# Kernel optimization log

Measured on AMD Instinct MI355X. Metric: run time of the kernel, lower is better.

## Reference

```python
import jax, jax.numpy as jnp
import numpy as np


def _rbf_kernel(X, Z, variance, lengthscale):
    # K[n, r] = variance * exp(-||x_n - z_r||^2 / (2 * lengthscale^2))
    x2 = jnp.sum(X * X, axis=-1)[:, None]          # [N, 1]
    z2 = jnp.sum(Z * Z, axis=-1)[None, :]          # [1, R]
    sq = x2 + z2 - 2.0 * (X @ Z.T)                 # [N, R]
    sq = jnp.maximum(sq, 0.0)
    return variance * jnp.exp(-0.5 * sq / (lengthscale * lengthscale))


def setup_inputs() -> dict:
    key = jax.random.key(0)
    ks = jax.random.split(key, 6)
    N, D, S, F, R = 16384, 8, 8, 1024, 2048
    X_star = jax.random.normal(ks[0], (N, D), dtype=jnp.float32)
    ref_points = jax.random.normal(ks[1], (R, D), dtype=jnp.float32)
    omega = jax.random.normal(ks[2], (S, D, F), dtype=jnp.float32)
    two_pi = 2.0 * np.pi
    phase = jax.random.uniform(ks[3], (S, F), dtype=jnp.float32) * two_pi
    feature_weights = jax.random.normal(ks[4], (S, F), dtype=jnp.float32)
    correction_weights = jax.random.normal(ks[5], (S, R), dtype=jnp.float32)
    variance = jnp.ones((), dtype=jnp.float32)
    lengthscale = jnp.ones((), dtype=jnp.float32)
    return {
        "X_star": X_star,
        "ref_points": ref_points,
        "omega": omega,
        "phase": phase,
        "feature_weights": feature_weights,
        "correction_weights": correction_weights,
        "variance": variance,
        "lengthscale": lengthscale,
    }


def reference(X_star, ref_points, omega, phase, feature_weights,
              correction_weights, variance, lengthscale):
    F = omega.shape[-1]
    # RFF prior paths: angles [S, N, F]
    angles = jnp.einsum('nd,sdf->snf', X_star, omega) / lengthscale + phase[:, None, :]
    scale = jnp.sqrt(2.0 * variance / F)
    features = scale * jnp.cos(angles)                       # [S, N, F]
    prior = jnp.sum(features * feature_weights[:, None, :], axis=-1)  # [S, N]
    # Kernel correction term
    K_cross = _rbf_kernel(X_star, ref_points, variance, lengthscale)  # [N, R]
    update = jnp.einsum('nr,sr->sn', K_cross, correction_weights)     # [S, N]
    # mean_fn is None -> zero mean
    mean = jnp.zeros(X_star.shape[0], dtype=X_star.dtype)
    return prior + update + mean[None, :]
```

## Files before the change

kernel.cpp:

```cpp
#include <hip/hip_runtime.h>
#include <math.h>

#ifndef __has_builtin
#define __has_builtin(x) 0
#endif

typedef __attribute__((ext_vector_type(8))) short bf16x8;
typedef __attribute__((ext_vector_type(4))) float f32x4;

__device__ __forceinline__ float fast_fract(float x) {
#if __has_builtin(__builtin_amdgcn_fractf)
    return __builtin_amdgcn_fractf(x);
#else
    return x - floorf(x);
#endif
}
__device__ __forceinline__ float fast_cos2pi(float x) {
#if __has_builtin(__builtin_amdgcn_cosf)
    return __builtin_amdgcn_cosf(x);
#else
    return cosf(x * 6.28318530717958647692f);
#endif
}
__device__ __forceinline__ float fast_exp2(float x) {
#if __has_builtin(__builtin_amdgcn_exp2f)
    return __builtin_amdgcn_exp2f(x);
#else
    return exp2f(x);
#endif
}
__device__ __forceinline__ unsigned short f2bf(float f) {
    unsigned u = __float_as_uint(f);
    return (unsigned short)((u + 0x7FFFu + ((u >> 16) & 1u)) >> 16);
}
__device__ __forceinline__ float bf2f(unsigned short b) {
    return __uint_as_float(((unsigned)b) << 16);
}
__device__ __forceinline__ unsigned packbf(float lo, float hi) {
    return (unsigned)f2bf(lo) | ((unsigned)f2bf(hi) << 16);
}

constexpr int kN = 16384, kD = 8, kS = 8, kF = 1024, kR = 2048;
constexpr float kInv2Pi = 0.15915494309189535f;
constexpr float kLog2e  = 1.4426950408889634f;
constexpr int kWsPrior = 512, kWsZ = 128, kWsCw = 64;
constexpr int kWsTiles = kWsPrior + kWsZ + kWsCw;
constexpr size_t kWsNeed = (size_t)kWsTiles * 64 * 16;

__global__ __launch_bounds__(256)
void prep_kernel(const float* __restrict__ omega, const float* __restrict__ phase,
                 const float* __restrict__ Z, const float* __restrict__ cw,
                 const float* __restrict__ lsp, uint4* __restrict__ ws,
                 float* __restrict__ out)
{
    if (blockIdx.x >= 176) {
        const int zid = (blockIdx.x - 176) * 256 + threadIdx.x;
        float4* o4 = reinterpret_cast<float4*>(out);
        #pragma unroll
        for (int j = 0; j < 4; ++j)
            o4[zid * 4 + j] = (float4){0.f, 0.f, 0.f, 0.f};
        return;
    }
    const int job  = blockIdx.x * 256 + threadIdx.x;
    const int lane = job & 63;
    const int tile = job >> 6;
    const int g = lane >> 4, c = lane & 15;

    const float inv_ls = 1.0f / lsp[0];
    const float m_ang  = kInv2Pi * inv_ls;
    const float L      = kLog2e * inv_ls * inv_ls;

    unsigned short h[8];
    if (tile < kWsPrior) {
        const int s = tile >> 6, ft = tile & 63, f = ft * 16 + c;
        const float* om = omega + s * (kD * kF);
        const float* ph = phase + s * kF;
        #pragma unroll
        for (int j = 0; j < 8; ++j) {
            const int k = g * 8 + j;
            unsigned short v = 0;
            if (k < 16) {
                v = f2bf(om[(k & 7) * kF + f] * m_ang);
            } else if (k < 24) {
                const float w = om[(k - 16) * kF + f] * m_ang;
                v = f2bf(w - bf2f(f2bf(w)));
            } else if (k == 24) {
                v = f2bf(ph[f] * kInv2Pi);
            } else if (k == 25) {
                const float p = ph[f] * kInv2Pi;
                v = f2bf(p - bf2f(f2bf(p)));
            }
            h[j] = v;
        }
    } else if (tile < kWsPrior + kWsZ) {
        const int rt = tile - kWsPrior;
        const int r  = rt * 16 + c;
        const float* zr = Z + r * kD;
        float zz = 0.f;
        #pragma unroll
        for (int d = 0; d < kD; ++d) zz = fmaf(zr[d], zr[d], zz);
        const float ztv = -0.5f * L * zz;
        #pragma unroll
        for (int j = 0; j < 8; ++j) {
            const int k = g * 8 + j;
            unsigned short v = 0;
            if (k < 8) {
                v = f2bf(L * zr[k]);
            } else if (k < 16) {
                v = f2bf(L * zr[k - 8]);
            } else if (k < 24) {
                const float w = L * zr[k - 16];
                v = f2bf(w - bf2f(f2bf(w)));
            } else if (k == 24) {
                v = f2bf(ztv);
            } else if (k == 25) {
                v = f2bf(ztv - bf2f(f2bf(ztv)));
            } else if (k < 28) {
                v = 0x3F80;
            }
            h[j] = v;
        }
    } else {
        const int rb = tile - kWsPrior - kWsZ;
        const int r0 = rb * 32;
        #pragma unroll
        for (int j = 0; j < 8; ++j)
            h[j] = (c < 8) ? f2bf(cw[c * kR + r0 + g * 8 + j]) : (unsigned short)0;
    }
    uint4 w;
    w.x = (unsigned)h[0] | ((unsigned)h[1] << 16);
    w.y = (unsigned)h[2] | ((unsigned)h[3] << 16);
    w.z = (unsigned)h[4] | ((unsigned)h[5] << 16);
    w.w = (unsigned)h[6] | ((unsigned)h[7] << 16);
    ws[tile * 64 + lane] = w;
}

__device__ __forceinline__ bf16x8 build_af_x(const float* __restrict__ X,
                                             int row, int g)
{
    float xv[kD];
    const float4 x0 = *reinterpret_cast<const float4*>(X + row * kD);
    const float4 x1 = *reinterpret_cast<const float4*>(X + row * kD + 4);
    xv[0]=x0.x; xv[1]=x0.y; xv[2]=x0.z; xv[3]=x0.w;
    xv[4]=x1.x; xv[5]=x1.y; xv[6]=x1.z; xv[7]=x1.w;
    bf16x8 af;
    if (g == 1) {
        #pragma unroll
        for (int j = 0; j < 8; ++j)
            af[j] = (short)f2bf(xv[j] - bf2f(f2bf(xv[j])));
    } else {
        #pragma unroll
        for (int j = 0; j < 8; ++j) af[j] = (short)f2bf(xv[j]);
    }
    return af;
}

__global__ __launch_bounds__(256, 6)
void fused_main(const float* __restrict__ X, const float* __restrict__ fw,
                const float* __restrict__ varp, const float* __restrict__ lsp,
                const uint4* __restrict__ wsP, const uint4* __restrict__ wsZ,
                const uint4* __restrict__ wsC, float* __restrict__ out)
{
    __shared__ unsigned b2raw[4][256];
    __shared__ f32x4 red[2][2][2][16];
    const int tid  = threadIdx.x;
    const int lane = tid & 63;
    const int w    = __builtin_amdgcn_readfirstlane(tid >> 6);
    const int c = lane & 15, g = lane >> 4;
    const int bid = blockIdx.x;
    const int btype = bid % 3;

    if (btype != 2) {
        const int pb = (bid / 3) * 2 + btype;
        const int s  = pb & 7;
        const int ng = pb >> 3;
        const int n0 = ng * 128 + w * 32;

        bf16x8 af0, af1;
        if (g == 3) {
            #pragma unroll
            for (int j = 0; j < 8; ++j) { af0[j] = 0; af1[j] = 0; }
            af0[0] = (short)0x3F80; af0[1] = (short)0x3F80;
            af1[0] = (short)0x3F80; af1[1] = (short)0x3F80;
        } else {
            af0 = build_af_x(X, n0 + c, g);
            af1 = build_af_x(X, n0 + 16 + c, g);
        }

        const float scale = sqrtf(2.0f * varp[0] / (float)kF);
        const uint4* bp  = wsP + s * 4096 + lane;
        const float* fwp = fw + s * kF + c;

        float acc[2][4];
        #pragma unroll
        for (int t = 0; t < 2; ++t)
            #pragma unroll
            for (int r = 0; r < 4; ++r) acc[t][r] = 0.f;

        uint4 b0 = bp[0], b1 = bp[64];
        f32x4 pd00, pd01, pd10, pd11;
        {
            const bf16x8 v0 = __builtin_bit_cast(bf16x8, b0);
            const bf16x8 v1 = __builtin_bit_cast(bf16x8, b1);
            pd00 = __builtin_amdgcn_mfma_f32_16x16x32_bf16(af0, v0, (f32x4){0.f,0.f,0.f,0.f}, 0, 0, 0);
            pd01 = __builtin_amdgcn_mfma_f32_16x16x32_bf16(af1, v0, (f32x4){0.f,0.f,0.f,0.f}, 0, 0, 0);
            pd10 = __builtin_amdgcn_mfma_f32_16x16x32_bf16(af0, v1, (f32x4){0.f,0.f,0.f,0.f}, 0, 0, 0);
            pd11 = __builtin_amdgcn_mfma_f32_16x16x32_bf16(af1, v1, (f32x4){0.f,0.f,0.f,0.f}, 0, 0, 0);
        }
        float cf0 = fwp[0], cf1 = fwp[16];
        b0 = bp[128]; b1 = bp[192];

        for (int it = 1; it < 32; ++it) {
            const int nx = (it + 1 < 32) ? it + 1 : it;
            const uint4 p0 = bp[nx * 128];
            const uint4 p1 = bp[nx * 128 + 64];
            const float nf0 = fwp[it * 32];
            const float nf1 = fwp[it * 32 + 16];
            const bf16x8 v0 = __builtin_bit_cast(bf16x8, b0);
            const bf16x8 v1 = __builtin_bit_cast(bf16x8, b1);
            const f32x4 nd00 = __builtin_amdgcn_mfma_f32_16x16x32_bf16(af0, v0, (f32x4){0.f,0.f,0.f,0.f}, 0, 0, 0);
            const f32x4 nd01 = __builtin_amdgcn_mfma_f32_16x16x32_bf16(af1, v0, (f32x4){0.f,0.f,0.f,0.f}, 0, 0, 0);
            const f32x4 nd10 = __builtin_amdgcn_mfma_f32_16x16x32_bf16(af0, v1, (f32x4){0.f,0.f,0.f,0.f}, 0, 0, 0);
            const f32x4 nd11 = __builtin_amdgcn_mfma_f32_16x16x32_bf16(af1, v1, (f32x4){0.f,0.f,0.f,0.f}, 0, 0, 0);
            #pragma unroll
            for (int r = 0; r < 4; ++r) {
                acc[0][r] = fmaf(cf0, fast_cos2pi(fast_fract(pd00[r])), acc[0][r]);
                acc[1][r] = fmaf(cf0, fast_cos2pi(fast_fract(pd01[r])), acc[1][r]);
                acc[0][r] = fmaf(cf1, fast_cos2pi(fast_fract(pd10[r])), acc[0][r]);
                acc[1][r] = fmaf(cf1, fast_cos2pi(fast_fract(pd11[r])), acc[1][r]);
            }
            pd00 = nd00; pd01 = nd01; pd10 = nd10; pd11 = nd11;
            cf0 = nf0; cf1 = nf1;
            b0 = p0; b1 = p1;
        }
        #pragma unroll
        for (int r = 0; r < 4; ++r) {
            acc[0][r] = fmaf(cf0, fast_cos2pi(fast_fract(pd00[r])), acc[0][r]);
            acc[1][r] = fmaf(cf0, fast_cos2pi(fast_fract(pd01[r])), acc[1][r]);
            acc[0][r] = fmaf(cf1, fast_cos2pi(fast_fract(pd10[r])), acc[0][r]);
            acc[1][r] = fmaf(cf1, fast_cos2pi(fast_fract(pd11[r])), acc[1][r]);
        }

        #pragma unroll
        for (int m = 1; m <= 8; m <<= 1)
            #pragma unroll
            for (int t = 0; t < 2; ++t)
                #pragma unroll
                for (int r = 0; r < 4; ++r)
                    acc[t][r] += __shfl_xor(acc[t][r], m);

        if (c == 0) {
            #pragma unroll
            for (int t = 0; t < 2; ++t) {
                float* o = out + s * kN + n0 + t * 16 + g * 4;
                #pragma unroll
                for (int r = 0; r < 4; ++r) atomicAdd(o + r, scale * acc[t][r]);
            }
        }
    } else {
        const int ub   = bid / 3;
        const int tl   = w >> 1, half = w & 1;
        const int n0   = (ub * 2 + tl) * 16;

        const float inv_ls = 1.0f / lsp[0];
        const float L = kLog2e * inv_ls * inv_ls;

        bf16x8 bf1;
        {
            float xv[kD];
            const float4 x0 = *reinterpret_cast<const float4*>(X + (n0 + c) * kD);
            const float4 x1 = *reinterpret_cast<const float4*>(X + (n0 + c) * kD + 4);
            xv[0]=x0.x; xv[1]=x0.y; xv[2]=x0.z; xv[3]=x0.w;
            xv[4]=x1.x; xv[5]=x1.y; xv[6]=x1.z; xv[7]=x1.w;
            if (g == 3) {
                float xx = 0.f;
                #pragma unroll
                for (int d = 0; d < kD; ++d) xx = fmaf(xv[d], xv[d], xx);
                const float xt = -0.5f * L * xx;
                const unsigned short th = f2bf(xt);
                const unsigned short tlw = f2bf(xt - bf2f(th));
                #pragma unroll
                for (int j = 0; j < 8; ++j) bf1[j] = 0;
                bf1[0] = (short)0x3F80; bf1[1] = (short)0x3F80;
                bf1[2] = (short)th;     bf1[3] = (short)tlw;
            } else if (g == 1) {
                #pragma unroll
                for (int j = 0; j < 8; ++j)
                    bf1[j] = (short)f2bf(xv[j] - bf2f(f2bf(xv[j])));
            } else {
                #pragma unroll
                for (int j = 0; j < 8; ++j) bf1[j] = (short)f2bf(xv[j]);
            }
        }

        const int wbase = (g >> 1) * 64 + c * 4 + (g & 1) * 2;
        const int rbase = (g >> 1) * 128 + (g & 1) * 64 + c * 4;
        unsigned* bb = &b2raw[w][0];

        const uint4* zp = wsZ + lane;
        const uint4* cp = wsC + lane;
        const int rb0 = half * 32;

        f32x4 acc = {0.f, 0.f, 0.f, 0.f};
        uint4 za = zp[(rb0 * 2) * 64];
        uint4 zb = zp[(rb0 * 2 + 1) * 64];
        uint4 cf = cp[rb0 * 64];

        for (int i = 0; i < 32; ++i) {
            const int rb = rb0 + i;
            const int rbn = (i < 31) ? rb + 1 : rb;
            const uint4 zan = zp[(rbn * 2) * 64];
            const uint4 zbn = zp[(rbn * 2 + 1) * 64];
            const uint4 cfn = cp[rbn * 64];

            const f32x4 e0 = __builtin_amdgcn_mfma_f32_16x16x32_bf16(
                __builtin_bit_cast(bf16x8, za), bf1, (f32x4){0.f,0.f,0.f,0.f}, 0, 0, 0);
            const f32x4 e1 = __builtin_amdgcn_mfma_f32_16x16x32_bf16(
                __builtin_bit_cast(bf16x8, zb), bf1, (f32x4){0.f,0.f,0.f,0.f}, 0, 0, 0);

            float K0[4], K1[4];
            #pragma unroll
            for (int r = 0; r < 4; ++r) {
                K0[r] = fast_exp2(fminf(e0[r], 0.f));
                K1[r] = fast_exp2(fminf(e1[r], 0.f));
            }
            uint2 w0; w0.x = packbf(K0[0], K0[1]); w0.y = packbf(K0[2], K0[3]);
            uint2 w1; w1.x = packbf(K1[0], K1[1]); w1.y = packbf(K1[2], K1[3]);
            *reinterpret_cast<uint2*>(&bb[wbase])       = w0;
            *reinterpret_cast<uint2*>(&bb[wbase + 128]) = w1;
            asm volatile("" ::: "memory");
            const uint4 b2w = *reinterpret_cast<const uint4*>(&bb[rbase]);
            asm volatile("" ::: "memory");

            acc = __builtin_amdgcn_mfma_f32_16x16x32_bf16(
                __builtin_bit_cast(bf16x8, cf), __builtin_bit_cast(bf16x8, b2w),
                acc, 0, 0, 0);

            za = zan; zb = zbn; cf = cfn;
        }

        if (g < 2) red[tl][half][g][c] = acc;
        __syncthreads();

        {
            const int tl2 = tid >> 7, s = (tid >> 4) & 7, n = tid & 15;
            const float sum = red[tl2][0][s >> 2][n][s & 3]
                            + red[tl2][1][s >> 2][n][s & 3];
            const int idx = s * kN + (ub * 2 + tl2) * 16 + n;
            atomicAdd(out + idx, varp[0] * sum);
        }
    }
}

__global__ __launch_bounds__(512, 8)
void prior_fb(const float* __restrict__ X, const float* __restrict__ omega,
              const float* __restrict__ phase, const float* __restrict__ fw,
              const float* __restrict__ varp, const float* __restrict__ lsp,
              float* __restrict__ out)
{
    const int tid  = threadIdx.x;
    const int nloc = tid & 63;
    const int wave = __builtin_amdgcn_readfirstlane(tid >> 6);
    const int s    = blockIdx.y;
    const int n    = blockIdx.x * 64 + nloc;
    const float variance = varp[0];
    const float inv_ls   = 1.0f / lsp[0];
    const float scale = sqrtf(2.0f * variance / (float)kF);
    float xa[kD];
    {
        const float4 x0 = *reinterpret_cast<const float4*>(X + n * kD);
        const float4 x1 = *reinterpret_cast<const float4*>(X + n * kD + 4);
        const float m = inv_ls * kInv2Pi;
        xa[0]=x0.x*m; xa[1]=x0.y*m; xa[2]=x0.z*m; xa[3]=x0.w*m;
        xa[4]=x1.x*m; xa[5]=x1.y*m; xa[6]=x1.z*m; xa[7]=x1.w*m;
    }
    const float* om  = omega + s * (kD * kF);
    const float* ph  = phase + s * kF;
    const float* fwp = fw    + s * kF;
    const int f0 = wave * 128;
    float acc0 = 0.f, acc1 = 0.f;
    for (int fb = f0; fb < f0 + 128; fb += 8) {
        float cv[8];
        #pragma unroll
        for (int j = 0; j < 8; ++j) {
            float t = ph[fb + j] * kInv2Pi;
            #pragma unroll
            for (int d = 0; d < kD; ++d) t = fmaf(xa[d], om[d * kF + fb + j], t);
            cv[j] = fast_cos2pi(fast_fract(t));
        }
        #pragma unroll
        for (int j = 0; j < 8; j += 2) {
            acc0 = fmaf(fwp[fb + j], cv[j], acc0);
            acc1 = fmaf(fwp[fb + j + 1], cv[j + 1], acc1);
        }
    }
    __shared__ float red[8][64];
    red[wave][nloc] = acc0 + acc1;
    __syncthreads();
    if (tid < 64) {
        float t = 0.f;
        #pragma unroll
        for (int k = 0; k < 8; ++k) t += red[k][tid];
        out[s * kN + blockIdx.x * 64 + tid] = scale * t;
    }
}

__global__ __launch_bounds__(1024, 8)
void update_fb(const float* __restrict__ X, const float* __restrict__ Z,
               const float* __restrict__ cw, const float* __restrict__ varp,
               const float* __restrict__ lsp, float* __restrict__ out)
{
    const int tid  = threadIdx.x;
    const int nloc = tid & 63;
    const int wave = __builtin_amdgcn_readfirstlane(tid >> 6);
    const int n    = blockIdx.x * 64 + nloc;
    const float variance = varp[0];
    const float inv_ls   = 1.0f / lsp[0];
    const float L = kLog2e * inv_ls * inv_ls;
    __shared__ float zt_lds[kR];
    __shared__ float red[16][64][kS + 1];
    float x[kD];
    {
        const float4 x0 = *reinterpret_cast<const float4*>(X + n * kD);
        const float4 x1 = *reinterpret_cast<const float4*>(X + n * kD + 4);
        x[0]=x0.x; x[1]=x0.y; x[2]=x0.z; x[3]=x0.w;
        x[4]=x1.x; x[5]=x1.y; x[6]=x1.z; x[7]=x1.w;
    }
    for (int r = tid; r < kR; r += 1024) {
        const float4 z0 = *reinterpret_cast<const float4*>(Z + r * kD);
        const float4 z1 = *reinterpret_cast<const float4*>(Z + r * kD + 4);
        float z2 = z0.x*z0.x + z0.y*z0.y + z0.z*z0.z + z0.w*z0.w
                 + z1.x*z1.x + z1.y*z1.y + z1.z*z1.z + z1.w*z1.w;
        zt_lds[r] = -0.5f * L * z2;
    }
    __syncthreads();
    float xb[kD]; float x2 = 0.f;
    #pragma unroll
    for (int d = 0; d < kD; ++d) { xb[d] = x[d] * L; x2 = fmaf(x[d], x[d], x2); }
    const float xt = -0.5f * L * x2;
    float accU[2][kS];
    #pragma unroll
    for (int j = 0; j < kS; ++j) { accU[0][j] = 0.f; accU[1][j] = 0.f; }
    const int r0 = wave * 128;
    #pragma unroll 4
    for (int rr = 0; rr < 128; ++rr) {
        const int r = r0 + rr;
        float e = xt + zt_lds[r];
        #pragma unroll
        for (int d = 0; d < kD; ++d) e = fmaf(xb[d], Z[r * kD + d], e);
        e = fminf(e, 0.f);
        const float K = fast_exp2(e);
        #pragma unroll
        for (int j = 0; j < kS; ++j)
            accU[rr & 1][j] = fmaf(K, cw[j * kR + r], accU[rr & 1][j]);
    }
    #pragma unroll
    for (int j = 0; j < kS; ++j) red[wave][nloc][j] = accU[0][j] + accU[1][j];
    __syncthreads();
    if (tid < 512) {
        const int n2 = tid & 63;
        const int jj = tid >> 6;
        float tot = 0.f;
        #pragma unroll
        for (int k = 0; k < 16; ++k) tot += red[k][n2][jj];
        const int idx = jj * kN + blockIdx.x * 64 + n2;
        out[idx] = fmaf(variance, tot, out[idx]);
    }
}

extern "C" void kernel_launch(void* const* d_in, const int* in_sizes, int n_in,
                              void* d_out, int out_size, void* d_ws, size_t ws_size,
                              hipStream_t stream) {
    const float* X  = (const float*)d_in[0];
    const float* Z  = (const float*)d_in[1];
    const float* om = (const float*)d_in[2];
    const float* ph = (const float*)d_in[3];
    const float* fw = (const float*)d_in[4];
    const float* cw = (const float*)d_in[5];
    const float* vp = (const float*)d_in[6];
    const float* lp = (const float*)d_in[7];
    float* out = (float*)d_out;

    if (ws_size >= kWsNeed) {
        uint4* wsP = (uint4*)d_ws;
        uint4* wsZ = wsP + (size_t)kWsPrior * 64;
        uint4* wsC = wsP + (size_t)(kWsPrior + kWsZ) * 64;
        hipLaunchKernelGGL(prep_kernel, dim3(208), dim3(256), 0, stream,
                           om, ph, Z, cw, lp, wsP, out);
        hipLaunchKernelGGL(fused_main, dim3(1536), dim3(256), 0, stream,
                           X, fw, vp, lp, wsP, wsZ, wsC, out);
    } else {
        hipLaunchKernelGGL(prior_fb, dim3(kN / 64, kS), dim3(512), 0, stream,
                           X, om, ph, fw, vp, lp, out);
        hipLaunchKernelGGL(update_fb, dim3(kN / 64), dim3(1024), 0, stream,
                           X, Z, cw, vp, lp, out);
    }
}
```

Baseline: 100.9 us.

## Double-buffer LDS kernel tile and lag the correction MFMA by one iteration

Software-pipelines the RBF correction loop: each iteration computes and stores the exp-kernel tile into one of two LDS buffers while the accumulation MFMA consumes the tile written in the previous iteration. This is meant to hide the LDS write-then-read latency and the dependency chain between the exp evaluation and the accumulate MFMA. It doubles the per-wave LDS scratch and adds a prologue and epilogue, which could slightly reduce occupancy or raise register pressure.

```diff
diff --git a/kernel.cpp b/kernel.cpp
--- a/kernel.cpp
+++ b/kernel.cpp
@@ -161,7 +161,7 @@
                 const uint4* __restrict__ wsP, const uint4* __restrict__ wsZ,
                 const uint4* __restrict__ wsC, float* __restrict__ out)
 {
-    __shared__ unsigned b2raw[4][256];
+    __shared__ unsigned b2raw[4][512];
     __shared__ f32x4 red[2][2][2][16];
     const int tid  = threadIdx.x;
     const int lane = tid & 63;
@@ -304,15 +304,41 @@
         f32x4 acc = {0.f, 0.f, 0.f, 0.f};
         uint4 za = zp[(rb0 * 2) * 64];
         uint4 zb = zp[(rb0 * 2 + 1) * 64];
-        uint4 cf = cp[rb0 * 64];
-
-        for (int i = 0; i < 32; ++i) {
+        uint4 cf_cur = cp[rb0 * 64];
+        uint4 cf_prev = cf_cur;
+
+        {
+            const uint4 zan = zp[((rb0 + 1) * 2) * 64];
+            const uint4 zbn = zp[((rb0 + 1) * 2 + 1) * 64];
+            const uint4 cfn = cp[(rb0 + 1) * 64];
+            const f32x4 e0 = __builtin_amdgcn_mfma_f32_16x16x32_bf16(
+                __builtin_bit_cast(bf16x8, za), bf1, (f32x4){0.f,0.f,0.f,0.f}, 0, 0, 0);
+            const f32x4 e1 = __builtin_amdgcn_mfma_f32_16x16x32_bf16(
+                __builtin_bit_cast(bf16x8, zb), bf1, (f32x4){0.f,0.f,0.f,0.f}, 0, 0, 0);
+            float K0[4], K1[4];
+            #pragma unroll
+            for (int r = 0; r < 4; ++r) {
+                K0[r] = fast_exp2(fminf(e0[r], 0.f));
+                K1[r] = fast_exp2(fminf(e1[r], 0.f));
+            }
+            uint2 w0; w0.x = packbf(K0[0], K0[1]); w0.y = packbf(K0[2], K0[3]);
+            uint2 w1; w1.x = packbf(K1[0], K1[1]); w1.y = packbf(K1[2], K1[3]);
+            *reinterpret_cast<uint2*>(&bb[wbase])       = w0;
+            *reinterpret_cast<uint2*>(&bb[wbase + 128]) = w1;
+            asm volatile("" ::: "memory");
+            cf_prev = cf_cur; cf_cur = cfn; za = zan; zb = zbn;
+        }
+
+        for (int i = 1; i < 32; ++i) {
             const int rb = rb0 + i;
             const int rbn = (i < 31) ? rb + 1 : rb;
             const uint4 zan = zp[(rbn * 2) * 64];
             const uint4 zbn = zp[(rbn * 2 + 1) * 64];
             const uint4 cfn = cp[rbn * 64];
 
+            const uint4 kprev = *reinterpret_cast<const uint4*>(
+                &bb[rbase + ((i - 1) & 1) * 256]);
+
             const f32x4 e0 = __builtin_amdgcn_mfma_f32_16x16x32_bf16(
                 __builtin_bit_cast(bf16x8, za), bf1, (f32x4){0.f,0.f,0.f,0.f}, 0, 0, 0);
             const f32x4 e1 = __builtin_amdgcn_mfma_f32_16x16x32_bf16(
@@ -326,17 +352,23 @@
             }
             uint2 w0; w0.x = packbf(K0[0], K0[1]); w0.y = packbf(K0[2], K0[3]);
             uint2 w1; w1.x = packbf(K1[0], K1[1]); w1.y = packbf(K1[2], K1[3]);
-            *reinterpret_cast<uint2*>(&bb[wbase])       = w0;
-            *reinterpret_cast<uint2*>(&bb[wbase + 128]) = w1;
+            *reinterpret_cast<uint2*>(&bb[wbase + (i & 1) * 256])       = w0;
+            *reinterpret_cast<uint2*>(&bb[wbase + 128 + (i & 1) * 256]) = w1;
             asm volatile("" ::: "memory");
-            const uint4 b2w = *reinterpret_cast<const uint4*>(&bb[rbase]);
-            asm volatile("" ::: "memory");
 
             acc = __builtin_amdgcn_mfma_f32_16x16x32_bf16(
-                __builtin_bit_cast(bf16x8, cf), __builtin_bit_cast(bf16x8, b2w),
+                __builtin_bit_cast(bf16x8, cf_prev), __builtin_bit_cast(bf16x8, kprev),
                 acc, 0, 0, 0);
 
-            za = zan; zb = zbn; cf = cfn;
+            cf_prev = cf_cur; cf_cur = cfn; za = zan; zb = zbn;
+        }
+
+        {
+            const uint4 kprev = *reinterpret_cast<const uint4*>(
+                &bb[rbase + (31 & 1) * 256]);
+            acc = __builtin_amdgcn_mfma_f32_16x16x32_bf16(
+                __builtin_bit_cast(bf16x8, cf_prev), __builtin_bit_cast(bf16x8, kprev),
+                acc, 0, 0, 0);
         }
 
         if (g < 2) red[tl][half][g][c] = acc;
```

Result: no change. 100.1 us (-0.8%).
